# Performance work log

Hardware: AMD Instinct MI355X
Metric: run time of the kernel (lower is better)

The kernel has to match this reference:

```python
import jax, jax.numpy as jnp
import numpy as np

MIN_TAU = 0.1
MAX_TAU = 10.0
DT = 0.1
HID = 64
IND = 3
B, N = 4, 262144


def _xavier(key, shape):
    fan_in, fan_out = shape[1], shape[0]
    limit = float(np.sqrt(6.0 / (fan_in + fan_out)))
    return jax.random.uniform(key, shape, jnp.float32, -limit, limit)


def setup_inputs() -> dict:
    key = jax.random.key(0)
    ks = jax.random.split(key, 7)
    h = jax.random.normal(ks[0], (B, N, HID), jnp.float32)
    u = jax.random.normal(ks[1], (B, N, IND), jnp.float32)
    return {
        "h": h,
        "u": u,
        "W_h": _xavier(ks[2], (HID, HID)),
        "U_h": _xavier(ks[3], (HID, IND)),
        "b_h": jnp.zeros((HID,), jnp.float32),
        "W_tau": _xavier(ks[4], (HID, HID)),
        "U_tau": _xavier(ks[5], (HID, IND)),
        "b_tau": jnp.zeros((HID,), jnp.float32),
        "W_out": _xavier(ks[6], (3, HID)),
        "b_out": jnp.zeros((3,), jnp.float32),
    }


def reference(h, u, W_h, U_h, b_h, W_tau, U_tau, b_tau, W_out, b_out):
    # tau: state-dependent time constant (B,N,HID)
    tau_raw = jnp.einsum('bnh,kh->bnk', h, W_tau) + jnp.einsum('bni,ki->bnk', u, U_tau) + b_tau
    tau = MIN_TAU + jax.nn.softplus(tau_raw) * (MAX_TAU - MIN_TAU)
    pre = jnp.einsum('bnh,kh->bnk', h, W_h) + jnp.einsum('bni,ki->bnk', u, U_h) + b_h
    f_h = jax.nn.sigmoid(pre)
    h_new = h + DT * (-h / tau + f_h)
    v = jnp.tanh(jnp.einsum('bnh,oh->bno', h_new, W_out) + b_out)
    return (h_new, v)
```

## Files before the change

### kernel.cpp

```cpp
#include <hip/hip_runtime.h>
#include <hip/hip_bf16.h>
#include <math.h>

#define HID 64
#define DT 0.1f
#define MIN_TAU 0.1f
#define TAU_SCALE 9.9f

#define WSTRIDE 104
#define WROWS   128
#define WELEMS  (WROWS * WSTRIDE)

typedef __attribute__((ext_vector_type(8))) short bf16x8;
typedef __attribute__((ext_vector_type(4))) float f32x4;

__device__ __forceinline__ short f2bf(float f) {
    union { __hip_bfloat16 b; short s; } c;
    c.b = __float2bfloat16(f);
    return c.s;
}
__device__ __forceinline__ float fast_rcp(float x) { return __builtin_amdgcn_rcpf(x); }
__device__ __forceinline__ float fast_tanh(float x) {
    float e = __expf(2.f * x);
    return fmaf(-2.f, fast_rcp(e + 1.f), 1.f);
}

__global__ __launch_bounds__(256) void prep_weights(
    const float* __restrict__ W_tau, const float* __restrict__ U_tau,
    const float* __restrict__ b_tau,
    const float* __restrict__ W_h, const float* __restrict__ U_h,
    const float* __restrict__ b_h,
    short* __restrict__ wbf)
{
    const int idx = blockIdx.x * 256 + threadIdx.x;
    if (idx >= WELEMS) return;
    const int row = idx / WSTRIDE;
    const int c = idx - row * WSTRIDE;
    float val = 0.f;
    if (row < 64) {
        const int r = row;
        if (c < 64)       val = W_tau[r * 64 + c];
        else if (c < 67)  val = U_tau[r * 3 + (c - 64)];
        else if (c == 67) val = b_tau[r];
    } else {
        const int r = row - 64;
        if (c < 64)       val = W_h[r * 64 + c];
        else if (c < 67)  val = U_h[r * 3 + (c - 64)];
        else if (c == 67) val = b_h[r];
    }
    wbf[idx] = f2bf(val);
}

__global__ __launch_bounds__(256, 2) void liquid_mfma_kernel(
    const float* __restrict__ h, const float* __restrict__ u,
    const short* __restrict__ wbf,
    const float* __restrict__ W_out, const float* __restrict__ b_out,
    float* __restrict__ h_out, float* __restrict__ v_out, int ntiles)
{
    const int tid  = threadIdx.x;
    const int lane = tid & 63;
    const int col  = lane & 15;
    const int quad = lane >> 4;
    const int wid  = tid >> 6;

    bf16x8 bw[8][3];
#pragma unroll
    for (int nt = 0; nt < 8; ++nt)
#pragma unroll
        for (int ks = 0; ks < 3; ++ks)
            bw[nt][ks] = *(const bf16x8*)&wbf[(nt * 16 + col) * WSTRIDE + ks * 32 + quad * 8];

    bf16x8 idA, idB;
#pragma unroll
    for (int e = 0; e < 8; ++e) {
        idA[e] = (quad * 8 + e == col)      ? (short)0x3F80 : (short)0;
        idB[e] = (quad * 8 + e == col + 16) ? (short)0x3F80 : (short)0;
    }

    float wo[3][4];
#pragma unroll
    for (int o = 0; o < 3; ++o)
#pragma unroll
        for (int nt = 0; nt < 4; ++nt)
            wo[o][nt] = W_out[o * 64 + nt * 16 + col];
    const float bo_sel = (col == 0) ? b_out[0] : ((col == 1) ? b_out[1] : b_out[2]);

    const int tstep = gridDim.x;
    int t = blockIdx.x;

    float4 pf0, pf1, pf2, pf3;
    float pu0 = 0.f, pu1 = 0.f, pu2 = 0.f;

#define LOADA(TT)                                                              \
    do {                                                                       \
        const unsigned q_ = (unsigned)(TT) * 64u + (unsigned)(wid * 16 + col); \
        const float* hp_ = h + q_ * 64u + (unsigned)(quad * 8);                \
        pf0 = *(const float4*)hp_;                                             \
        pf1 = *(const float4*)(hp_ + 4);                                       \
        pf2 = *(const float4*)(hp_ + 32);                                      \
        pf3 = *(const float4*)(hp_ + 36);                                      \
        if (quad == 0) {                                                       \
            const float* up_ = u + q_ * 3u;                                    \
            pu0 = up_[0]; pu1 = up_[1]; pu2 = up_[2];                          \
        }                                                                      \
    } while (0)

    if (t < ntiles) LOADA(t);

    for (; t < ntiles; t += tstep) {
        const unsigned q0 = (unsigned)t * 64u + (unsigned)(wid * 16);

        bf16x8 af0, af1;
        af0[0] = f2bf(pf0.x); af0[1] = f2bf(pf0.y); af0[2] = f2bf(pf0.z); af0[3] = f2bf(pf0.w);
        af0[4] = f2bf(pf1.x); af0[5] = f2bf(pf1.y); af0[6] = f2bf(pf1.z); af0[7] = f2bf(pf1.w);
        af1[0] = f2bf(pf2.x); af1[1] = f2bf(pf2.y); af1[2] = f2bf(pf2.z); af1[3] = f2bf(pf2.w);
        af1[4] = f2bf(pf3.x); af1[5] = f2bf(pf3.y); af1[6] = f2bf(pf3.z); af1[7] = f2bf(pf3.w);

        bf16x8 af2 = (bf16x8)(short)0;
        if (quad == 0) {
            af2[0] = f2bf(pu0); af2[1] = f2bf(pu1); af2[2] = f2bf(pu2);
            af2[3] = f2bf(1.0f);
        }

        const int tn = t + tstep;
        if (tn < ntiles) LOADA(tn);

        f32x4 acc[12];
#pragma unroll
        for (int nt = 0; nt < 12; ++nt) acc[nt] = (f32x4){0.f, 0.f, 0.f, 0.f};

#pragma unroll
        for (int nt = 0; nt < 8; ++nt) {
            acc[nt] = __builtin_amdgcn_mfma_f32_16x16x32_bf16(af0, bw[nt][0], acc[nt], 0, 0, 0);
            acc[nt] = __builtin_amdgcn_mfma_f32_16x16x32_bf16(af1, bw[nt][1], acc[nt], 0, 0, 0);
            acc[nt] = __builtin_amdgcn_mfma_f32_16x16x32_bf16(af2, bw[nt][2], acc[nt], 0, 0, 0);
        }
        acc[8]  = __builtin_amdgcn_mfma_f32_16x16x32_bf16(af0, idA, acc[8],  0, 0, 0);
        acc[9]  = __builtin_amdgcn_mfma_f32_16x16x32_bf16(af0, idB, acc[9],  0, 0, 0);
        acc[10] = __builtin_amdgcn_mfma_f32_16x16x32_bf16(af1, idA, acc[10], 0, 0, 0);
        acc[11] = __builtin_amdgcn_mfma_f32_16x16x32_bf16(af1, idB, acc[11], 0, 0, 0);

#pragma unroll
        for (int r = 0; r < 4; ++r) {
            const unsigned p = q0 + (unsigned)(quad * 4 + r);
            float pv0 = 0.f, pv1 = 0.f, pv2 = 0.f;
#pragma unroll
            for (int ntk = 0; ntk < 4; ++ntk) {
                const float at = acc[ntk][r];
                const float ap = acc[ntk + 4][r];
                const float hk = acc[ntk + 8][r];
                const float sp = fmaxf(at, 0.f) + __logf(1.f + __expf(-fabsf(at)));
                const float tau = fmaf(sp, TAU_SCALE, MIN_TAU);
                const float f = fast_rcp(1.f + __expf(-ap));
                const float hnew = fmaf(DT, f - hk * fast_rcp(tau), hk);
                h_out[p * 64u + (unsigned)(ntk * 16 + col)] = hnew;
                pv0 = fmaf(hnew, wo[0][ntk], pv0);
                pv1 = fmaf(hnew, wo[1][ntk], pv1);
                pv2 = fmaf(hnew, wo[2][ntk], pv2);
            }
#pragma unroll
            for (int s = 1; s < 16; s <<= 1) {
                pv0 += __shfl_xor(pv0, s, 64);
                pv1 += __shfl_xor(pv1, s, 64);
                pv2 += __shfl_xor(pv2, s, 64);
            }
            const float pv = (col == 0) ? pv0 : ((col == 1) ? pv1 : pv2);
            if (col < 3)
                v_out[p * 3u + (unsigned)col] = fast_tanh(pv + bo_sel);
        }
    }
#undef LOADA
}

extern "C" void kernel_launch(void* const* d_in, const int* in_sizes, int n_in,
                              void* d_out, int out_size, void* d_ws, size_t ws_size,
                              hipStream_t stream) {
    const float* h     = (const float*)d_in[0];
    const float* u     = (const float*)d_in[1];
    const float* W_h   = (const float*)d_in[2];
    const float* U_h   = (const float*)d_in[3];
    const float* b_h   = (const float*)d_in[4];
    const float* W_tau = (const float*)d_in[5];
    const float* U_tau = (const float*)d_in[6];
    const float* b_tau = (const float*)d_in[7];
    const float* W_out = (const float*)d_in[8];
    const float* b_out = (const float*)d_in[9];

    const int total = in_sizes[0] / HID;
    float* h_out = (float*)d_out;
    float* v_out = h_out + (size_t)total * HID;

    short* wbf = (short*)d_ws;

    prep_weights<<<(WELEMS + 255) / 256, 256, 0, stream>>>(
        W_tau, U_tau, b_tau, W_h, U_h, b_h, wbf);

    const int ntiles = total / 64;
    const int grid = 1024;
    liquid_mfma_kernel<<<grid, 256, 0, stream>>>(
        h, u, wbf, W_out, b_out, h_out, v_out, ntiles);
}
```

Baseline: 140.2 us.

## Stage bf16 weights in LDS and split accumulation to raise occupancy

Weights stop living in registers (24 bf16x8 per lane) and are copied once per block into shared memory, then read from LDS for each MFMA. The accumulation is split into two halves over output columns, so fewer accumulators are live at once. Launch bounds go from 2 to 4 blocks per CU to raise occupancy for this memory-bound kernel. The cost is added LDS reads per tile, possible bank conflicts, and about 26KB of LDS per block, which may itself limit occupancy.

After: 272.7 us. 1.95x slower.

```diff
diff --git a/kernel.cpp b/kernel.cpp
--- a/kernel.cpp
+++ b/kernel.cpp
@@ -51,25 +51,26 @@
     wbf[idx] = f2bf(val);
 }
 
-__global__ __launch_bounds__(256, 2) void liquid_mfma_kernel(
+__global__ __launch_bounds__(256, 4) void liquid_mfma_kernel(
     const float* __restrict__ h, const float* __restrict__ u,
     const short* __restrict__ wbf,
     const float* __restrict__ W_out, const float* __restrict__ b_out,
     float* __restrict__ h_out, float* __restrict__ v_out, int ntiles)
 {
-    const int tid  = threadIdx.x;
+    __shared__ short wlds[WELEMS];
+
+    const int tid = threadIdx.x;
+    {
+        const uint4* s = (const uint4*)wbf;
+        uint4* d = (uint4*)wlds;
+        for (int i = tid; i < WELEMS / 8; i += 256) d[i] = s[i];
+    }
+
     const int lane = tid & 63;
     const int col  = lane & 15;
     const int quad = lane >> 4;
     const int wid  = tid >> 6;
 
-    bf16x8 bw[8][3];
-#pragma unroll
-    for (int nt = 0; nt < 8; ++nt)
-#pragma unroll
-        for (int ks = 0; ks < 3; ++ks)
-            bw[nt][ks] = *(const bf16x8*)&wbf[(nt * 16 + col) * WSTRIDE + ks * 32 + quad * 8];
-
     bf16x8 idA, idB;
 #pragma unroll
     for (int e = 0; e < 8; ++e) {
@@ -84,6 +85,10 @@
         for (int nt = 0; nt < 4; ++nt)
             wo[o][nt] = W_out[o * 64 + nt * 16 + col];
     const float bo_sel = (col == 0) ? b_out[0] : ((col == 1) ? b_out[1] : b_out[2]);
+
+    __syncthreads();
+
+    const short* wbase = &wlds[col * WSTRIDE + quad * 8];
 
     const int tstep = gridDim.x;
     int t = blockIdx.x;
@@ -125,48 +130,70 @@
         const int tn = t + tstep;
         if (tn < ntiles) LOADA(tn);
 
-        f32x4 acc[12];
-#pragma unroll
-        for (int nt = 0; nt < 12; ++nt) acc[nt] = (f32x4){0.f, 0.f, 0.f, 0.f};
-
-#pragma unroll
-        for (int nt = 0; nt < 8; ++nt) {
-            acc[nt] = __builtin_amdgcn_mfma_f32_16x16x32_bf16(af0, bw[nt][0], acc[nt], 0, 0, 0);
-            acc[nt] = __builtin_amdgcn_mfma_f32_16x16x32_bf16(af1, bw[nt][1], acc[nt], 0, 0, 0);
-            acc[nt] = __builtin_amdgcn_mfma_f32_16x16x32_bf16(af2, bw[nt][2], acc[nt], 0, 0, 0);
+        float pv[4][3];
+#pragma unroll
+        for (int r = 0; r < 4; ++r) { pv[r][0] = 0.f; pv[r][1] = 0.f; pv[r][2] = 0.f; }
+
+#pragma unroll
+        for (int H = 0; H < 2; ++H) {
+            const f32x4 z = (f32x4){0.f, 0.f, 0.f, 0.f};
+            f32x4 aT0 = z, aT1 = z, aP0 = z, aP1 = z, aH0 = z, aH1 = z;
+
+            const short* wT0 = wbase + (H * 2 + 0) * 16 * WSTRIDE;
+            const short* wT1 = wbase + (H * 2 + 1) * 16 * WSTRIDE;
+            const short* wP0 = wbase + (4 + H * 2) * 16 * WSTRIDE;
+            const short* wP1 = wbase + (5 + H * 2) * 16 * WSTRIDE;
+
+            aT0 = __builtin_amdgcn_mfma_f32_16x16x32_bf16(af0, *(const bf16x8*)(wT0),      aT0, 0, 0, 0);
+            aT0 = __builtin_amdgcn_mfma_f32_16x16x32_bf16(af1, *(const bf16x8*)(wT0 + 32), aT0, 0, 0, 0);
+            aT0 = __builtin_amdgcn_mfma_f32_16x16x32_bf16(af2, *(const bf16x8*)(wT0 + 64), aT0, 0, 0, 0);
+            aT1 = __builtin_amdgcn_mfma_f32_16x16x32_bf16(af0, *(const bf16x8*)(wT1),      aT1, 0, 0, 0);
+            aT1 = __builtin_amdgcn_mfma_f32_16x16x32_bf16(af1, *(const bf16x8*)(wT1 + 32), aT1, 0, 0, 0);
+            aT1 = __builtin_amdgcn_mfma_f32_16x16x32_bf16(af2, *(const bf16x8*)(wT1 + 64), aT1, 0, 0, 0);
+            aP0 = __builtin_amdgcn_mfma_f32_16x16x32_bf16(af0, *(const bf16x8*)(wP0),      aP0, 0, 0, 0);
+            aP0 = __builtin_amdgcn_mfma_f32_16x16x32_bf16(af1, *(const bf16x8*)(wP0 + 32), aP0, 0, 0, 0);
+            aP0 = __builtin_amdgcn_mfma_f32_16x16x32_bf16(af2, *(const bf16x8*)(wP0 + 64), aP0, 0, 0, 0);
+            aP1 = __builtin_amdgcn_mfma_f32_16x16x32_bf16(af0, *(const bf16x8*)(wP1),      aP1, 0, 0, 0);
+            aP1 = __builtin_amdgcn_mfma_f32_16x16x32_bf16(af1, *(const bf16x8*)(wP1 + 32), aP1, 0, 0, 0);
+            aP1 = __builtin_amdgcn_mfma_f32_16x16x32_bf16(af2, *(const bf16x8*)(wP1 + 64), aP1, 0, 0, 0);
+            const bf16x8 afid = H ? af1 : af0;
+            aH0 = __builtin_amdgcn_mfma_f32_16x16x32_bf16(afid, idA, aH0, 0, 0, 0);
+            aH1 = __builtin_amdgcn_mfma_f32_16x16x32_bf16(afid, idB, aH1, 0, 0, 0);
+
+#pragma unroll
+            for (int r = 0; r < 4; ++r) {
+                const unsigned p = q0 + (unsigned)(quad * 4 + r);
+#pragma unroll
+                for (int j = 0; j < 2; ++j) {
+                    const int ntk = H * 2 + j;
+                    const float at = j ? aT1[r] : aT0[r];
+                    const float ap = j ? aP1[r] : aP0[r];
+                    const float hk = j ? aH1[r] : aH0[r];
+                    const float sp = fmaxf(at, 0.f) + __logf(1.f + __expf(-fabsf(at)));
+                    const float tau = fmaf(sp, TAU_SCALE, MIN_TAU);
+                    const float f = fast_rcp(1.f + __expf(-ap));
+                    const float hnew = fmaf(DT, f - hk * fast_rcp(tau), hk);
+                    h_out[p * 64u + (unsigned)(ntk * 16 + col)] = hnew;
+                    pv[r][0] = fmaf(hnew, wo[0][ntk], pv[r][0]);
+                    pv[r][1] = fmaf(hnew, wo[1][ntk], pv[r][1]);
+                    pv[r][2] = fmaf(hnew, wo[2][ntk], pv[r][2]);
+                }
+            }
         }
-        acc[8]  = __builtin_amdgcn_mfma_f32_16x16x32_bf16(af0, idA, acc[8],  0, 0, 0);
-        acc[9]  = __builtin_amdgcn_mfma_f32_16x16x32_bf16(af0, idB, acc[9],  0, 0, 0);
-        acc[10] = __builtin_amdgcn_mfma_f32_16x16x32_bf16(af1, idA, acc[10], 0, 0, 0);
-        acc[11] = __builtin_amdgcn_mfma_f32_16x16x32_bf16(af1, idB, acc[11], 0, 0, 0);
 
 #pragma unroll
         for (int r = 0; r < 4; ++r) {
             const unsigned p = q0 + (unsigned)(quad * 4 + r);
-            float pv0 = 0.f, pv1 = 0.f, pv2 = 0.f;
-#pragma unroll
-            for (int ntk = 0; ntk < 4; ++ntk) {
-                const float at = acc[ntk][r];
-                const float ap = acc[ntk + 4][r];
-                const float hk = acc[ntk + 8][r];
-                const float sp = fmaxf(at, 0.f) + __logf(1.f + __expf(-fabsf(at)));
-                const float tau = fmaf(sp, TAU_SCALE, MIN_TAU);
-                const float f = fast_rcp(1.f + __expf(-ap));
-                const float hnew = fmaf(DT, f - hk * fast_rcp(tau), hk);
-                h_out[p * 64u + (unsigned)(ntk * 16 + col)] = hnew;
-                pv0 = fmaf(hnew, wo[0][ntk], pv0);
-                pv1 = fmaf(hnew, wo[1][ntk], pv1);
-                pv2 = fmaf(hnew, wo[2][ntk], pv2);
-            }
+            float pv0 = pv[r][0], pv1 = pv[r][1], pv2 = pv[r][2];
 #pragma unroll
             for (int s = 1; s < 16; s <<= 1) {
                 pv0 += __shfl_xor(pv0, s, 64);
                 pv1 += __shfl_xor(pv1, s, 64);
                 pv2 += __shfl_xor(pv2, s, 64);
             }
-            const float pv = (col == 0) ? pv0 : ((col == 1) ? pv1 : pv2);
+            const float pvs = (col == 0) ? pv0 : ((col == 1) ? pv1 : pv2);
             if (col < 3)
-                v_out[p * 3u + (unsigned)col] = fast_tanh(pv + bo_sel);
+                v_out[p * 3u + (unsigned)col] = fast_tanh(pvs + bo_sel);
         }
     }
 #undef LOADA
```
